# Performance work log

Hardware: AMD Instinct MI355X
Metric: run time of the kernel (lower is better)

Reference implementation:

```python
import jax, jax.numpy as jnp
import numpy as np

BATCH = 2
SEQ = 2048
DIM = 2048
HEADS = 16
DIM_HEAD = 64
DIM_INNER = HEADS * DIM_HEAD  # 1024
SOFTCAP = 50.0
EPS = 1e-12


def setup_inputs() -> dict:
    key = jax.random.key(0)
    k1, k2, k3, k4 = jax.random.split(key, 4)
    x = jax.random.normal(k1, (BATCH, SEQ, DIM), dtype=jnp.float32)
    # RMSNorm gamma param (initialized near zero in the torch module)
    gamma = jax.random.normal(k2, (DIM,), dtype=jnp.float32) * 0.02
    # Linear weights stored already-transposed: x @ W
    w_qkv = jax.random.normal(k3, (DIM, 3 * DIM_INNER), dtype=jnp.float32) * (DIM ** -0.5)
    w_out = jax.random.normal(k4, (DIM_INNER, DIM), dtype=jnp.float32) * (DIM_INNER ** -0.5)
    # (type, offset, length) triples per batch; bidirectional attention inside each span
    modalities = jnp.array(
        [[[0, 256, 256], [0, 1024, 512]],
         [[0, 128, 256], [0, 1536, 384]]], dtype=jnp.int32)
    return dict(x=x, gamma=gamma, w_qkv=w_qkv, w_out=w_out, modalities=modalities)


def _transfusion_attn_mask(seq_len, modalities):
    # causal | (q in span AND kv in span)  -> Bool[b, i, j]
    seq = jnp.arange(seq_len)
    causal = seq[:, None] >= seq[None, :]                      # [i, j]
    offsets = modalities[..., 1]                                # [b, m]
    ends = offsets + modalities[..., 2]                         # [b, m]
    q_in = seq[None, None, :] >= offsets[..., None]             # [b, m, i]
    kv_in = seq[None, None, :] < ends[..., None]                # [b, m, j]
    is_modality = jnp.any(q_in[..., :, None] & kv_in[..., None, :], axis=1)  # [b, i, j]
    return causal[None] | is_modality


def _rmsnorm(x, gamma):
    n = jnp.sqrt(jnp.sum(x * x, axis=-1, keepdims=True))
    x = x / jnp.maximum(n, EPS)
    return x * (DIM ** 0.5) * (gamma + 1.0)


def reference(x, gamma, w_qkv, w_out, modalities):
    xn = _rmsnorm(x, gamma)
    qkv = xn @ w_qkv                                            # [b, n, 3*h*d]
    qkv = qkv.reshape(BATCH, SEQ, 3, HEADS, DIM_HEAD)
    qkv = jnp.transpose(qkv, (2, 0, 3, 1, 4))                   # [3, b, h, n, d]
    q, k, v = qkv[0], qkv[1], qkv[2]
    q = q * (DIM_HEAD ** -0.5)
    sim = jnp.einsum('bhid,bhjd->bhij', q, k)
    sim = jnp.tanh(sim / SOFTCAP) * SOFTCAP                     # softclamp
    mask = _transfusion_attn_mask(SEQ, modalities)              # [b, i, j]
    neg = -jnp.finfo(sim.dtype).max
    sim = jnp.where(mask[:, None, :, :], sim, neg)
    attn = jax.nn.softmax(sim, axis=-1)
    out = jnp.einsum('bhij,bhjd->bhid', attn, v)
    out = jnp.transpose(out, (0, 2, 1, 3)).reshape(BATCH, SEQ, DIM_INNER)
    return out @ w_out
```

## Files before the change

kernel.cpp:

```cpp
#include <hip/hip_runtime.h>
#include <hip/hip_bf16.h>

typedef unsigned short u16;
typedef unsigned int u32;
typedef __attribute__((ext_vector_type(8))) short short8;
typedef __attribute__((ext_vector_type(4))) float f32x4;
typedef __attribute__((ext_vector_type(4))) u16 u16x4;

#define DEV __device__ __forceinline__

DEV u16 f2bf(float f) {
    union { float f; u32 u; } v; v.f = f;
    u32 r = v.u;
    u32 lsb = (r >> 16) & 1u;
    r += 0x7fffu + lsb;
    return (u16)(r >> 16);
}

DEV void gload_lds16(const u16* g, u16* l) {
    __builtin_amdgcn_global_load_lds(
        (const __attribute__((address_space(1))) u32*)(const void*)g,
        (__attribute__((address_space(3))) u32*)(void*)l,
        16, 0, 0);
}

__global__ void transpose_cast(const float* __restrict__ in, u16* __restrict__ out,
                               int R, int C) {
    __shared__ float tile[32][33];
    int c0 = blockIdx.x * 32, r0 = blockIdx.y * 32;
    int tx = threadIdx.x, ty = threadIdx.y;
#pragma unroll
    for (int i = 0; i < 4; i++)
        tile[ty * 4 + i][tx] = in[(size_t)(r0 + ty * 4 + i) * C + c0 + tx];
    __syncthreads();
#pragma unroll
    for (int i = 0; i < 4; i++)
        out[(size_t)(c0 + ty * 4 + i) * R + r0 + tx] = f2bf(tile[tx][ty * 4 + i]);
}

__global__ void rmsnorm_cast(const float* __restrict__ x, const float* __restrict__ gamma,
                             u16* __restrict__ xn) {
    int row = blockIdx.x;
    int t = threadIdx.x;
    const float4* xr = (const float4*)(x + (size_t)row * 2048);
    float4 a = xr[t];
    float4 b = xr[256 + t];
    float ss = a.x * a.x + a.y * a.y + a.z * a.z + a.w * a.w +
               b.x * b.x + b.y * b.y + b.z * b.z + b.w * b.w;
#pragma unroll
    for (int off = 32; off; off >>= 1) ss += __shfl_xor(ss, off);
    __shared__ float red[4];
    if ((t & 63) == 0) red[t >> 6] = ss;
    __syncthreads();
    float tot = red[0] + red[1] + red[2] + red[3];
    float n = sqrtf(tot);
    float inv = 45.254833995939045f / fmaxf(n, 1e-12f);
    const float4* gr = (const float4*)gamma;
    float4 g0 = gr[t], g1 = gr[256 + t];
    u16x4 o0 = { f2bf(a.x * inv * (g0.x + 1.f)), f2bf(a.y * inv * (g0.y + 1.f)),
                 f2bf(a.z * inv * (g0.z + 1.f)), f2bf(a.w * inv * (g0.w + 1.f)) };
    u16x4 o1 = { f2bf(b.x * inv * (g1.x + 1.f)), f2bf(b.y * inv * (g1.y + 1.f)),
                 f2bf(b.z * inv * (g1.z + 1.f)), f2bf(b.w * inv * (g1.w + 1.f)) };
    u16x4* xo = (u16x4*)(xn + (size_t)row * 2048);
    xo[t] = o0;
    xo[256 + t] = o1;
}

template <int EPI>
__global__ __launch_bounds__(512, 1) void gemm8p(
    const u16* __restrict__ A, const u16* __restrict__ BT,
    int M, int N, int K, int nbx,
    float* __restrict__ Cout,
    u16* __restrict__ qb, u16* __restrict__ kb, u16* __restrict__ vT) {
    __shared__ __align__(16) u16 As[2][2][8192];
    __shared__ __align__(16) u16 Bs[2][2][8192];
    int t = threadIdx.x, lane = t & 63, wid = t >> 6;
    int g = lane >> 4, r = lane & 15;
    int wm = wid >> 2, wn = wid & 3;

    int nwg = gridDim.x;
    int id = blockIdx.x;
    int wg = (id & 7) * (nwg >> 3) + (id >> 3);
    int bx = wg % nbx, by = wg / nbx;
    int brow = by * 256, bcol = bx * 256;

    const u16* Ag = A + (size_t)(brow + (t >> 2)) * K + (t & 3) * 8;
    const u16* Bg = BT + (size_t)(bcol + (t >> 2)) * K + (t & 3) * 8;
    const size_t rstep = (size_t)128 * K;
    int dst0 = (t & ~63) * 8;
    int dst1 = 4096 + dst0;

    f32x4 acc[8][4] = {};
    int NT = K >> 6;

#define STG_A(bf_, kt_, kh_) { \
        gload_lds16(Ag + (kt_) * 64 + (kh_) * 32,         &As[bf_][kh_][dst0]); \
        gload_lds16(Ag + rstep + (kt_) * 64 + (kh_) * 32, &As[bf_][kh_][dst1]); }
#define STG_B(bf_, kt_, kh_) { \
        gload_lds16(Bg + (kt_) * 64 + (kh_) * 32,         &Bs[bf_][kh_][dst0]); \
        gload_lds16(Bg + rstep + (kt_) * 64 + (kh_) * 32, &Bs[bf_][kh_][dst1]); }

    STG_A(0, 0, 0); STG_B(0, 0, 0);
    STG_A(0, 0, 1); STG_B(0, 0, 1);
    STG_A(1, 1, 0); STG_B(1, 1, 0);
    asm volatile("s_waitcnt vmcnt(4)" ::: "memory");
    __builtin_amdgcn_s_barrier();

    for (int kt = 0; kt < NT; ++kt) {
        int buf = kt & 1, ob = buf ^ 1;
        const u16* Ak0 = As[buf][0];
        const u16* Ak1 = As[buf][1];
        const u16* Bk0 = Bs[buf][0];
        const u16* Bk1 = Bs[buf][1];
        bool s1 = kt + 1 < NT, s2 = kt + 2 < NT;
        short8 af[4], bfr[4];

#pragma unroll
        for (int n = 0; n < 4; n++)
            bfr[n] = *(const short8*)&Bk0[(wn * 64 + n * 16 + r) * 32 + g * 8];
#pragma unroll
        for (int m = 0; m < 4; m++)
            af[m] = *(const short8*)&Ak0[(wm * 128 + m * 16 + r) * 32 + g * 8];
        if (s1) STG_A(ob, kt + 1, 1);
        __builtin_amdgcn_s_barrier();
        asm volatile("s_waitcnt lgkmcnt(0)" ::: "memory");
        __builtin_amdgcn_s_setprio(1);
#pragma unroll
        for (int m = 0; m < 4; m++)
#pragma unroll
            for (int n = 0; n < 4; n++)
                acc[m][n] = __builtin_amdgcn_mfma_f32_16x16x32_bf16(af[m], bfr[n], acc[m][n], 0, 0, 0);
        __builtin_amdgcn_s_setprio(0);
        __builtin_amdgcn_s_barrier();

#pragma unroll
        for (int m = 0; m < 4; m++)
            af[m] = *(const short8*)&Ak0[(wm * 128 + 64 + m * 16 + r) * 32 + g * 8];
        if (s1) STG_B(ob, kt + 1, 1);
        __builtin_amdgcn_s_barrier();
        asm volatile("s_waitcnt lgkmcnt(0)" ::: "memory");
        __builtin_amdgcn_s_setprio(1);
#pragma unroll
        for (int m = 0; m < 4; m++)
#pragma unroll
            for (int n = 0; n < 4; n++)
                acc[4 + m][n] = __builtin_amdgcn_mfma_f32_16x16x32_bf16(af[m], bfr[n], acc[4 + m][n], 0, 0, 0);
        __builtin_amdgcn_s_setprio(0);
        __builtin_amdgcn_s_barrier();

#pragma unroll
        for (int n = 0; n < 4; n++)
            bfr[n] = *(const short8*)&Bk1[(wn * 64 + n * 16 + r) * 32 + g * 8];
#pragma unroll
        for (int m = 0; m < 4; m++)
            af[m] = *(const short8*)&Ak1[(wm * 128 + m * 16 + r) * 32 + g * 8];
        if (s2) STG_A(buf, kt + 2, 0);
        __builtin_amdgcn_s_barrier();
        asm volatile("s_waitcnt lgkmcnt(0)" ::: "memory");
        __builtin_amdgcn_s_setprio(1);
#pragma unroll
        for (int m = 0; m < 4; m++)
#pragma unroll
            for (int n = 0; n < 4; n++)
                acc[m][n] = __builtin_amdgcn_mfma_f32_16x16x32_bf16(af[m], bfr[n], acc[m][n], 0, 0, 0);
        __builtin_amdgcn_s_setprio(0);
        __builtin_amdgcn_s_barrier();

#pragma unroll
        for (int m = 0; m < 4; m++)
            af[m] = *(const short8*)&Ak1[(wm * 128 + 64 + m * 16 + r) * 32 + g * 8];
        if (s2) STG_B(buf, kt + 2, 0);
        __builtin_amdgcn_s_barrier();
        asm volatile("s_waitcnt lgkmcnt(0)" ::: "memory");
        __builtin_amdgcn_s_setprio(1);
#pragma unroll
        for (int m = 0; m < 4; m++)
#pragma unroll
            for (int n = 0; n < 4; n++)
                acc[4 + m][n] = __builtin_amdgcn_mfma_f32_16x16x32_bf16(af[m], bfr[n], acc[4 + m][n], 0, 0, 0);
        __builtin_amdgcn_s_setprio(0);
        if (s2)      { asm volatile("s_waitcnt vmcnt(4)" ::: "memory"); }
        else if (s1) { asm volatile("s_waitcnt vmcnt(0)" ::: "memory"); }
        __builtin_amdgcn_s_barrier();
    }
#undef STG_A
#undef STG_B

    if (EPI == 0) {
#pragma unroll
        for (int m = 0; m < 8; m++)
#pragma unroll
            for (int n = 0; n < 4; n++) {
                int cb = bcol + wn * 64 + n * 16 + r;
                int which = cb >> 10;
                int hd = cb & 1023;
                int hh = hd >> 6, d = hd & 63;
#pragma unroll
                for (int j = 0; j < 4; j++) {
                    int rr = brow + wm * 128 + m * 16 + 4 * g + j;
                    int b = rr >> 11, nn = rr & 2047;
                    float v = acc[m][n][j];
                    size_t bh = (size_t)(b * 16 + hh);
                    if (which == 0)      qb[(bh * 2048 + nn) * 64 + d] = f2bf(v * 0.125f);
                    else if (which == 1) kb[(bh * 2048 + nn) * 64 + d] = f2bf(v);
                    else                 vT[(bh * 64 + d) * 2048 + nn] = f2bf(v);
                }
            }
    } else {
#pragma unroll
        for (int m = 0; m < 8; m++)
#pragma unroll
            for (int n = 0; n < 4; n++) {
                int cb = bcol + wn * 64 + n * 16 + r;
#pragma unroll
                for (int j = 0; j < 4; j++) {
                    int rr = brow + wm * 128 + m * 16 + 4 * g + j;
                    Cout[(size_t)rr * N + cb] = acc[m][n][j];
                }
            }
    }
}

__global__ __launch_bounds__(256, 3) void flash_attn(
    const u16* __restrict__ q, const u16* __restrict__ kk, const u16* __restrict__ vT,
    const int* __restrict__ mods, u16* __restrict__ attn_out) {
    __shared__ __align__(16) u16 Ks[2][4096];
    __shared__ __align__(16) u16 Vs[2][4096];
    __shared__ __align__(16) u16 Plds[4][16][72];
    int t = threadIdx.x, lane = t & 63, wave = t >> 6;
    int g = lane >> 4, r = lane & 15;
    int h = blockIdx.x, b = blockIdx.y;
    int qs = (31 - blockIdx.z) * 64;
    int bh = b * 16 + h;
    int qbase = qs + wave * 16;

    int off0 = mods[b * 6 + 1], end0 = off0 + mods[b * 6 + 2];
    int off1 = mods[b * 6 + 4], end1 = off1 + mods[b * 6 + 5];

    const u16* Qp = q + ((size_t)bh * 2048 + qbase) * 64;
    short8 qf0 = *(const short8*)(Qp + (size_t)r * 64 + 8 * g);
    short8 qf1 = *(const short8*)(Qp + (size_t)r * 64 + 32 + 8 * g);

    int iq = qbase + r;
    int lim0 = (iq >= off0) ? end0 : 0;
    int lim1 = (iq >= off1) ? end1 : 0;
    int rowlim = max(iq + 1, max(lim0, lim1));

    int jlb = qs + 64;
    if (qs + 63 >= off0) jlb = max(jlb, end0);
    if (qs + 63 >= off1) jlb = max(jlb, end1);

    const u16* Kp = kk + (size_t)bh * 2048 * 64;
    const u16* Vp = vT + (size_t)bh * 64 * 2048;
    u16* Pw = &Plds[wave][0][0];

    f32x4 ot[4] = {};
    float psA = 0.f, psB = 0.f;
    int sw = r & 7;

    auto stage64 = [&](const u16* gbase, int gstride, u16* lds) {
#pragma unroll
        for (int i = 0; i < 2; i++) {
            int c = i * 256 + t;
            int row = c >> 3;
            int gsl = (c & 7) ^ (row & 7);
            gload_lds16(gbase + (size_t)row * gstride + 8 * gsl,
                        lds + (size_t)(c & ~63) * 8);
        }
    };

    stage64(Kp, 64, Ks[0]);
    stage64(Vp, 2048, Vs[0]);
    int buf = 0;

    for (int jb = 0; jb < jlb; jb += 64) {
        if (jb + 64 < jlb) {
            stage64(Kp + (size_t)(jb + 64) * 64, 64, Ks[buf ^ 1]);
            stage64(Vp + (jb + 64), 2048, Vs[buf ^ 1]);
            asm volatile("s_waitcnt vmcnt(4)" ::: "memory");
        } else {
            asm volatile("s_waitcnt vmcnt(0)" ::: "memory");
        }
        __builtin_amdgcn_s_barrier();
        const u16* Kt = Ks[buf];
        const u16* Vt = Vs[buf];

        f32x4 st[4];
#pragma unroll
        for (int tt = 0; tt < 4; tt++) {
            int row = 16 * tt + r;
            short8 kf0 = *(const short8*)&Kt[(size_t)(row * 8 + (g ^ sw)) * 8];
            short8 kf1 = *(const short8*)&Kt[(size_t)(row * 8 + ((4 + g) ^ sw)) * 8];
            f32x4 z = {};
            z = __builtin_amdgcn_mfma_f32_16x16x32_bf16(kf0, qf0, z, 0, 0, 0);
            z = __builtin_amdgcn_mfma_f32_16x16x32_bf16(kf1, qf1, z, 0, 0, 0);
            st[tt] = z;
        }
#pragma unroll
        for (int tt = 0; tt < 4; tt++) {
            int kvb = jb + 16 * tt + 4 * g;
            float p0, p1, p2, p3;
#pragma unroll
            for (int j = 0; j < 4; j++) {
                float x = st[tt][j];
                float x2 = x * x;
                float inner = __builtin_fmaf(x2, 2.1333333e-8f, -1.3333333e-4f);
                float poly = __builtin_fmaf(x2, inner, 1.0f);
                float pv = __expf(x * poly);
                pv = (kvb + j < rowlim) ? pv : 0.f;
                if (j == 0) p0 = pv; else if (j == 1) p1 = pv;
                else if (j == 2) p2 = pv; else p3 = pv;
            }
            psA += p0 + p1;
            psB += p2 + p3;
            u32 pk0, pk1;
            asm("v_cvt_pk_bf16_f32 %0, %1, %2" : "=v"(pk0) : "v"(p0), "v"(p1));
            asm("v_cvt_pk_bf16_f32 %0, %1, %2" : "=v"(pk1) : "v"(p2), "v"(p3));
            *(u32*)&Pw[r * 72 + 16 * tt + 4 * g] = pk0;
            *(u32*)&Pw[r * 72 + 16 * tt + 4 * g + 2] = pk1;
        }
        short8 pf0 = *(const short8*)&Pw[r * 72 + 8 * g];
        short8 pf1 = *(const short8*)&Pw[r * 72 + 32 + 8 * g];
#pragma unroll
        for (int dt = 0; dt < 4; dt++) {
            int row = 16 * dt + r;
            short8 vf0 = *(const short8*)&Vt[(size_t)(row * 8 + (g ^ sw)) * 8];
            short8 vf1 = *(const short8*)&Vt[(size_t)(row * 8 + ((4 + g) ^ sw)) * 8];
            ot[dt] = __builtin_amdgcn_mfma_f32_16x16x32_bf16(vf0, pf0, ot[dt], 0, 0, 0);
            ot[dt] = __builtin_amdgcn_mfma_f32_16x16x32_bf16(vf1, pf1, ot[dt], 0, 0, 0);
        }
        asm volatile("s_waitcnt lgkmcnt(0)" ::: "memory");
        __builtin_amdgcn_s_barrier();
        buf ^= 1;
    }

    float lrow = psA + psB;
    lrow += __shfl_xor(lrow, 16);
    lrow += __shfl_xor(lrow, 32);
    float inv = 1.f / lrow;
    u16* Op = attn_out + ((size_t)(b * 2048 + qbase + r)) * 1024 + h * 64;
#pragma unroll
    for (int dt = 0; dt < 4; dt++) {
        u16x4 o = { f2bf(ot[dt][0] * inv), f2bf(ot[dt][1] * inv),
                    f2bf(ot[dt][2] * inv), f2bf(ot[dt][3] * inv) };
        *(u16x4*)(Op + dt * 16 + 4 * g) = o;
    }
}

extern "C" void kernel_launch(void* const* d_in, const int* in_sizes, int n_in,
                              void* d_out, int out_size, void* d_ws, size_t ws_size,
                              hipStream_t stream) {
    const float* x = (const float*)d_in[0];
    const float* gamma = (const float*)d_in[1];
    const float* w_qkv = (const float*)d_in[2];
    const float* w_out = (const float*)d_in[3];
    const int* mods = (const int*)d_in[4];
    float* out = (float*)d_out;

    u16* ws = (u16*)d_ws;
    u16* xn    = ws;
    u16* wqkvT = ws + 8388608;
    u16* woutT = ws + 14680064;
    u16* qb    = ws + 16777216;
    u16* kb    = ws + 20971520;
    u16* vT    = ws + 25165824;
    u16* ao    = ws + 29360128;

    transpose_cast<<<dim3(96, 64), dim3(32, 8), 0, stream>>>(w_qkv, wqkvT, 2048, 3072);
    transpose_cast<<<dim3(64, 32), dim3(32, 8), 0, stream>>>(w_out, woutT, 1024, 2048);
    rmsnorm_cast<<<dim3(4096), dim3(256), 0, stream>>>(x, gamma, xn);
    gemm8p<0><<<dim3(192), dim3(512), 0, stream>>>(xn, wqkvT, 4096, 3072, 2048, 12,
                                                   nullptr, qb, kb, vT);
    flash_attn<<<dim3(16, 2, 32), dim3(256), 0, stream>>>(qb, kb, vT, mods, ao);
    gemm8p<1><<<dim3(128), dim3(512), 0, stream>>>(ao, woutT, 4096, 2048, 1024, 8,
                                                   out, nullptr, nullptr, nullptr);
}
```

Measured before the change: 195.9 us.

## Swizzle GEMM LDS layout and use 256x128 tiles for output projection

Adds an XOR swizzle on the k-chunk index for both the global-to-LDS staging and the LDS fragment reads, to cut LDS bank conflicts in the MFMA operand loads. The GEMM is also templated on the wave grid. The output projection now uses 256x128 tiles with a 4x2 wave layout, giving 256 workgroups instead of 128 so the machine has more tiles to spread across CUs. The cost is less operand reuse per tile and per-configuration wait counts that must stay correct.

```diff
diff --git a/kernel.cpp b/kernel.cpp
--- a/kernel.cpp
+++ b/kernel.cpp
@@ -66,44 +66,53 @@
     xo[256 + t] = o1;
 }
 
-template <int EPI>
+template <int EPI, int WM, int WN>
 __global__ __launch_bounds__(512, 1) void gemm8p(
     const u16* __restrict__ A, const u16* __restrict__ BT,
     int M, int N, int K, int nbx,
     float* __restrict__ Cout,
     u16* __restrict__ qb, u16* __restrict__ kb, u16* __restrict__ vT) {
+    constexpr int MF = 16 / WM;
+    constexpr int BN = WN * 64;
+    constexpr int BLB = BN / 128;
     __shared__ __align__(16) u16 As[2][2][8192];
-    __shared__ __align__(16) u16 Bs[2][2][8192];
+    __shared__ __align__(16) u16 Bs[2][2][BN * 32];
     int t = threadIdx.x, lane = t & 63, wid = t >> 6;
     int g = lane >> 4, r = lane & 15;
-    int wm = wid >> 2, wn = wid & 3;
+    int wm = wid / WN, wn = wid % WN;
+    int lin = (g ^ ((r >> 1) & 3)) * 8;
 
     int nwg = gridDim.x;
     int id = blockIdx.x;
     int wg = (id & 7) * (nwg >> 3) + (id >> 3);
     int bx = wg % nbx, by = wg / nbx;
-    int brow = by * 256, bcol = bx * 256;
-
-    const u16* Ag = A + (size_t)(brow + (t >> 2)) * K + (t & 3) * 8;
-    const u16* Bg = BT + (size_t)(bcol + (t >> 2)) * K + (t & 3) * 8;
+    int brow = by * 256, bcol = bx * BN;
+
+    int gk = (t & 3) ^ ((t >> 3) & 3);
+    const u16* Ag = A + (size_t)(brow + (t >> 2)) * K + gk * 8;
+    const u16* Bg = BT + (size_t)(bcol + (t >> 2)) * K + gk * 8;
     const size_t rstep = (size_t)128 * K;
     int dst0 = (t & ~63) * 8;
     int dst1 = 4096 + dst0;
 
-    f32x4 acc[8][4] = {};
+    f32x4 acc[MF][4] = {};
     int NT = K >> 6;
 
 #define STG_A(bf_, kt_, kh_) { \
         gload_lds16(Ag + (kt_) * 64 + (kh_) * 32,         &As[bf_][kh_][dst0]); \
         gload_lds16(Ag + rstep + (kt_) * 64 + (kh_) * 32, &As[bf_][kh_][dst1]); }
 #define STG_B(bf_, kt_, kh_) { \
-        gload_lds16(Bg + (kt_) * 64 + (kh_) * 32,         &Bs[bf_][kh_][dst0]); \
-        gload_lds16(Bg + rstep + (kt_) * 64 + (kh_) * 32, &Bs[bf_][kh_][dst1]); }
+        gload_lds16(Bg + (kt_) * 64 + (kh_) * 32, &Bs[bf_][kh_][dst0]); \
+        if constexpr (BLB == 2) \
+            gload_lds16(Bg + rstep + (kt_) * 64 + (kh_) * 32, &Bs[bf_][kh_][dst1]); }
+#define WAIT_INFLIGHT() { \
+        if constexpr (BLB == 2) { asm volatile("s_waitcnt vmcnt(4)" ::: "memory"); } \
+        else                    { asm volatile("s_waitcnt vmcnt(3)" ::: "memory"); } }
 
     STG_A(0, 0, 0); STG_B(0, 0, 0);
     STG_A(0, 0, 1); STG_B(0, 0, 1);
     STG_A(1, 1, 0); STG_B(1, 1, 0);
-    asm volatile("s_waitcnt vmcnt(4)" ::: "memory");
+    WAIT_INFLIGHT();
     __builtin_amdgcn_s_barrier();
 
     for (int kt = 0; kt < NT; ++kt) {
@@ -113,20 +122,20 @@
         const u16* Bk0 = Bs[buf][0];
         const u16* Bk1 = Bs[buf][1];
         bool s1 = kt + 1 < NT, s2 = kt + 2 < NT;
-        short8 af[4], bfr[4];
+        short8 af[MF / 2], bfr[4];
 
 #pragma unroll
         for (int n = 0; n < 4; n++)
-            bfr[n] = *(const short8*)&Bk0[(wn * 64 + n * 16 + r) * 32 + g * 8];
-#pragma unroll
-        for (int m = 0; m < 4; m++)
-            af[m] = *(const short8*)&Ak0[(wm * 128 + m * 16 + r) * 32 + g * 8];
+            bfr[n] = *(const short8*)&Bk0[(wn * 64 + n * 16 + r) * 32 + lin];
+#pragma unroll
+        for (int m = 0; m < MF / 2; m++)
+            af[m] = *(const short8*)&Ak0[(wm * (MF * 16) + m * 16 + r) * 32 + lin];
         if (s1) STG_A(ob, kt + 1, 1);
         __builtin_amdgcn_s_barrier();
         asm volatile("s_waitcnt lgkmcnt(0)" ::: "memory");
         __builtin_amdgcn_s_setprio(1);
 #pragma unroll
-        for (int m = 0; m < 4; m++)
+        for (int m = 0; m < MF / 2; m++)
 #pragma unroll
             for (int n = 0; n < 4; n++)
                 acc[m][n] = __builtin_amdgcn_mfma_f32_16x16x32_bf16(af[m], bfr[n], acc[m][n], 0, 0, 0);
@@ -134,32 +143,32 @@
         __builtin_amdgcn_s_barrier();
 
 #pragma unroll
-        for (int m = 0; m < 4; m++)
-            af[m] = *(const short8*)&Ak0[(wm * 128 + 64 + m * 16 + r) * 32 + g * 8];
+        for (int m = 0; m < MF / 2; m++)
+            af[m] = *(const short8*)&Ak0[(wm * (MF * 16) + (MF / 2) * 16 + m * 16 + r) * 32 + lin];
         if (s1) STG_B(ob, kt + 1, 1);
         __builtin_amdgcn_s_barrier();
         asm volatile("s_waitcnt lgkmcnt(0)" ::: "memory");
         __builtin_amdgcn_s_setprio(1);
 #pragma unroll
-        for (int m = 0; m < 4; m++)
+        for (int m = 0; m < MF / 2; m++)
 #pragma unroll
             for (int n = 0; n < 4; n++)
-                acc[4 + m][n] = __builtin_amdgcn_mfma_f32_16x16x32_bf16(af[m], bfr[n], acc[4 + m][n], 0, 0, 0);
+                acc[MF / 2 + m][n] = __builtin_amdgcn_mfma_f32_16x16x32_bf16(af[m], bfr[n], acc[MF / 2 + m][n], 0, 0, 0);
         __builtin_amdgcn_s_setprio(0);
         __builtin_amdgcn_s_barrier();
 
 #pragma unroll
         for (int n = 0; n < 4; n++)
-            bfr[n] = *(const short8*)&Bk1[(wn * 64 + n * 16 + r) * 32 + g * 8];
-#pragma unroll
-        for (int m = 0; m < 4; m++)
-            af[m] = *(const short8*)&Ak1[(wm * 128 + m * 16 + r) * 32 + g * 8];
+            bfr[n] = *(const short8*)&Bk1[(wn * 64 + n * 16 + r) * 32 + lin];
+#pragma unroll
+        for (int m = 0; m < MF / 2; m++)
+            af[m] = *(const short8*)&Ak1[(wm * (MF * 16) + m * 16 + r) * 32 + lin];
         if (s2) STG_A(buf, kt + 2, 0);
         __builtin_amdgcn_s_barrier();
         asm volatile("s_waitcnt lgkmcnt(0)" ::: "memory");
         __builtin_amdgcn_s_setprio(1);
 #pragma unroll
-        for (int m = 0; m < 4; m++)
+        for (int m = 0; m < MF / 2; m++)
 #pragma unroll
             for (int n = 0; n < 4; n++)
                 acc[m][n] = __builtin_amdgcn_mfma_f32_16x16x32_bf16(af[m], bfr[n], acc[m][n], 0, 0, 0);
@@ -167,28 +176,29 @@
         __builtin_amdgcn_s_barrier();
 
 #pragma unroll
-        for (int m = 0; m < 4; m++)
-            af[m] = *(const short8*)&Ak1[(wm * 128 + 64 + m * 16 + r) * 32 + g * 8];
+        for (int m = 0; m < MF / 2; m++)
+            af[m] = *(const short8*)&Ak1[(wm * (MF * 16) + (MF / 2) * 16 + m * 16 + r) * 32 + lin];
         if (s2) STG_B(buf, kt + 2, 0);
         __builtin_amdgcn_s_barrier();
         asm volatile("s_waitcnt lgkmcnt(0)" ::: "memory");
         __builtin_amdgcn_s_setprio(1);
 #pragma unroll
-        for (int m = 0; m < 4; m++)
+        for (int m = 0; m < MF / 2; m++)
 #pragma unroll
             for (int n = 0; n < 4; n++)
-                acc[4 + m][n] = __builtin_amdgcn_mfma_f32_16x16x32_bf16(af[m], bfr[n], acc[4 + m][n], 0, 0, 0);
+                acc[MF / 2 + m][n] = __builtin_amdgcn_mfma_f32_16x16x32_bf16(af[m], bfr[n], acc[MF / 2 + m][n], 0, 0, 0);
         __builtin_amdgcn_s_setprio(0);
-        if (s2)      { asm volatile("s_waitcnt vmcnt(4)" ::: "memory"); }
+        if (s2)      { WAIT_INFLIGHT(); }
         else if (s1) { asm volatile("s_waitcnt vmcnt(0)" ::: "memory"); }
         __builtin_amdgcn_s_barrier();
     }
 #undef STG_A
 #undef STG_B
+#undef WAIT_INFLIGHT
 
     if (EPI == 0) {
 #pragma unroll
-        for (int m = 0; m < 8; m++)
+        for (int m = 0; m < MF; m++)
 #pragma unroll
             for (int n = 0; n < 4; n++) {
                 int cb = bcol + wn * 64 + n * 16 + r;
@@ -197,7 +207,7 @@
                 int hh = hd >> 6, d = hd & 63;
 #pragma unroll
                 for (int j = 0; j < 4; j++) {
-                    int rr = brow + wm * 128 + m * 16 + 4 * g + j;
+                    int rr = brow + wm * (MF * 16) + m * 16 + 4 * g + j;
                     int b = rr >> 11, nn = rr & 2047;
                     float v = acc[m][n][j];
                     size_t bh = (size_t)(b * 16 + hh);
@@ -208,13 +218,13 @@
             }
     } else {
 #pragma unroll
-        for (int m = 0; m < 8; m++)
+        for (int m = 0; m < MF; m++)
 #pragma unroll
             for (int n = 0; n < 4; n++) {
                 int cb = bcol + wn * 64 + n * 16 + r;
 #pragma unroll
                 for (int j = 0; j < 4; j++) {
-                    int rr = brow + wm * 128 + m * 16 + 4 * g + j;
+                    int rr = brow + wm * (MF * 16) + m * 16 + 4 * g + j;
                     Cout[(size_t)rr * N + cb] = acc[m][n][j];
                 }
             }
@@ -369,9 +379,9 @@
     transpose_cast<<<dim3(96, 64), dim3(32, 8), 0, stream>>>(w_qkv, wqkvT, 2048, 3072);
     transpose_cast<<<dim3(64, 32), dim3(32, 8), 0, stream>>>(w_out, woutT, 1024, 2048);
     rmsnorm_cast<<<dim3(4096), dim3(256), 0, stream>>>(x, gamma, xn);
-    gemm8p<0><<<dim3(192), dim3(512), 0, stream>>>(xn, wqkvT, 4096, 3072, 2048, 12,
-                                                   nullptr, qb, kb, vT);
+    gemm8p<0, 2, 4><<<dim3(192), dim3(512), 0, stream>>>(xn, wqkvT, 4096, 3072, 2048, 12,
+                                                         nullptr, qb, kb, vT);
     flash_attn<<<dim3(16, 2, 32), dim3(256), 0, stream>>>(qb, kb, vT, mods, ao);
-    gemm8p<1><<<dim3(128), dim3(512), 0, stream>>>(ao, woutT, 4096, 2048, 1024, 8,
-                                                   out, nullptr, nullptr, nullptr);
-}
+    gemm8p<1, 4, 2><<<dim3(256), dim3(512), 0, stream>>>(ao, woutT, 4096, 2048, 1024, 16,
+                                                         out, nullptr, nullptr, nullptr);
+}
```

Measured after the change: 180.1 us. 8.1% less time.
